# Kernel optimization log

Hardware: AMD Instinct MI355X
Metric: run time of the kernel (lower is better)

## Reference

```python
import jax, jax.numpy as jnp
import numpy as np

N, M, NNZ = 100000, 20000, 1000000
IN_C, OUT_C, HEADS, FH = 128, 128, 4, 32  # FH = hidden_channels // heads
NEG_SLOPE = 0.2


def setup_inputs() -> dict:
    key = jax.random.key(0)
    ks = jax.random.split(key, 10)
    def glorot(k, shape):
        fan_in, fan_out = shape[-1], shape[-2] if len(shape) > 1 else shape[-1]
        s = jnp.sqrt(6.0 / (fan_in + fan_out))
        return jax.random.uniform(k, shape, jnp.float32, -s, s)
    return {
        "x": jax.random.normal(ks[0], (N, IN_C), jnp.float32),
        "hyperedge_attr": jax.random.normal(ks[1], (M, IN_C), jnp.float32),
        "lin1_W": glorot(ks[2], (HEADS * FH, IN_C)),
        "he_lin1_W": glorot(ks[3], (HEADS * FH, IN_C)),
        "att1": glorot(ks[4], (1, HEADS, 2 * FH)),
        "bias1": jnp.zeros((HEADS * FH,), jnp.float32),
        "lin2_W": glorot(ks[5], (OUT_C, HEADS * FH)),
        "bias2": jnp.zeros((OUT_C,), jnp.float32),
        "node_idx": jax.random.randint(ks[6], (NNZ,), 0, N),
        "edge_idx": jax.random.randint(ks[7], (NNZ,), 0, M),
    }


def _seg_softmax(logits, seg, num_seg):
    # segment-wise softmax over entries grouped by seg (PyG softmax)
    m = jax.ops.segment_max(logits, seg, num_segments=num_seg)
    m = jnp.where(jnp.isfinite(m), m, 0.0)  # empty segments
    e = jnp.exp(logits - m[seg])
    s = jax.ops.segment_sum(e, seg, num_segments=num_seg)
    return e / (s[seg] + 1e-16)


def reference(x, hyperedge_attr, lin1_W, he_lin1_W, att1, bias1, lin2_W, bias2,
              node_idx, edge_idx):
    n, m, nnz = x.shape[0], hyperedge_attr.shape[0], node_idx.shape[0]
    ones = jnp.ones((nnz,), x.dtype)
    deg = jax.ops.segment_sum(ones, node_idx, num_segments=n)      # D
    Dinv = jnp.where(deg > 0, 1.0 / deg, 0.0)
    bsz = jax.ops.segment_sum(ones, edge_idx, num_segments=m)      # B
    Binv = jnp.where(bsz > 0, 1.0 / bsz, 0.0)

    # ---- layer 1: attention conv, heads=4, concat ----
    x1 = (x @ lin1_W.T).reshape(n, HEADS, FH)                      # [N,H,F]
    he = (hyperedge_attr @ he_lin1_W.T).reshape(m, HEADS, FH)      # [M,H,F]
    a_i = (x1[node_idx] * att1[:, :, :FH]).sum(-1)                 # [nnz,H]
    a_j = (he[edge_idx] * att1[:, :, FH:]).sum(-1)
    alpha = jax.nn.leaky_relu(a_i + a_j, NEG_SLOPE)
    alpha = _seg_softmax(alpha, node_idx, n)                        # softmax per node

    # node -> hyperedge: B[e] * alpha * x1[node]
    msg = Binv[edge_idx][:, None, None] * x1[node_idx] * alpha[:, :, None]
    out_e = jax.ops.segment_sum(msg, edge_idx, num_segments=m)      # [M,H,F]
    # hyperedge -> node: D[v] * alpha * out_e[edge]
    msg = Dinv[node_idx][:, None, None] * out_e[edge_idx] * alpha[:, :, None]
    out_n = jax.ops.segment_sum(msg, node_idx, num_segments=n)      # [N,H,F]
    h = jax.nn.elu(out_n.reshape(n, HEADS * FH) + bias1)            # HCHA applies elu

    # ---- layer 2: plain conv (heads=1) ----
    x2 = h @ lin2_W.T                                               # [N,OUT_C]
    oe = jax.ops.segment_sum(Binv[edge_idx][:, None] * x2[node_idx],
                             edge_idx, num_segments=m)
    out = jax.ops.segment_sum(Dinv[node_idx][:, None] * oe[edge_idx],
                              node_idx, num_segments=n)
    return out + bias2
```

## Files before the change

kernel.cpp:

```cpp
#include <hip/hip_runtime.h>
#include <cstdint>


#define E_SHIFT 6
#define N_SHIFT 7
#define EB_CAP 4096
#define NB_CAP 2048
#define PCHUNK 4096
#define NBE_CAP 320
#define NBN_CAP 800

__device__ __forceinline__ unsigned wave_incl_scan(unsigned x) {
#pragma unroll
  for (int s = 1; s < 64; s <<= 1) {
    unsigned t = __shfl_up(x, s, 64);
    if ((int)(threadIdx.x & 63) >= s) x += t;
  }
  return x;
}

__global__ __launch_bounds__(256) void bucket_count(const int* __restrict__ node_idx,
                                                    const int* __restrict__ edge_idx,
                                                    unsigned* __restrict__ bcnt_e,
                                                    unsigned* __restrict__ bcnt_n, int nnz) {
  __shared__ unsigned he[NBE_CAP];
  __shared__ unsigned hn[NBN_CAP];
  const int t = threadIdx.x;
  const int base = blockIdx.x * PCHUNK;
  const int cnt = min(PCHUNK, nnz - base);
  for (int b = t; b < NBE_CAP; b += 256) he[b] = 0;
  for (int b = t; b < NBN_CAP; b += 256) hn[b] = 0;
  __syncthreads();
  for (int idx = t; idx < cnt; idx += 256) {
    unsigned e = (unsigned)edge_idx[base + idx];
    unsigned n = (unsigned)node_idx[base + idx];
    atomicAdd(&he[e >> E_SHIFT], 1u);
    atomicAdd(&hn[n >> N_SHIFT], 1u);
  }
  __syncthreads();
  for (int b = t; b < NBE_CAP; b += 256) if (he[b]) atomicAdd(&bcnt_e[b], he[b]);
  for (int b = t; b < NBN_CAP; b += 256) if (hn[b]) atomicAdd(&bcnt_n[b], hn[b]);
}

__global__ __launch_bounds__(1024) void bucket_scan(const unsigned* __restrict__ bcnt_e,
                                                    const unsigned* __restrict__ bcnt_n,
                                                    unsigned* __restrict__ bbase_e,
                                                    unsigned* __restrict__ bcur_e,
                                                    unsigned* __restrict__ bbase_n,
                                                    unsigned* __restrict__ bcur_n,
                                                    unsigned* __restrict__ eoff,
                                                    unsigned* __restrict__ noff,
                                                    int nbe, int nbn, int M_, int N_, int nnz) {
  __shared__ unsigned wsum[16];
  const int i = threadIdx.x;
  const int lane = i & 63, wid = i >> 6;
  {
    unsigned v = (i < nbe) ? bcnt_e[i] : 0u;
    unsigned incl = wave_incl_scan(v);
    if (lane == 63) wsum[wid] = incl;
    __syncthreads();
    unsigned add = 0;
    for (int w = 0; w < wid; ++w) add += wsum[w];
    unsigned excl = add + incl - v;
    if (i <= nbe) bbase_e[i] = excl;
    if (i < nbe) bcur_e[i] = excl;
    __syncthreads();
  }
  {
    unsigned v = (i < nbn) ? bcnt_n[i] : 0u;
    unsigned incl = wave_incl_scan(v);
    if (lane == 63) wsum[wid] = incl;
    __syncthreads();
    unsigned add = 0;
    for (int w = 0; w < wid; ++w) add += wsum[w];
    unsigned excl = add + incl - v;
    if (i <= nbn) bbase_n[i] = excl;
    if (i < nbn) bcur_n[i] = excl;
  }
  if (i == 0) { eoff[M_] = (unsigned)nnz; noff[N_] = (unsigned)nnz; }
}

__global__ __launch_bounds__(256) void partition2(const int* __restrict__ node_idx,
                                                  const int* __restrict__ edge_idx,
                                                  unsigned* __restrict__ bcur_e,
                                                  unsigned* __restrict__ bcur_n,
                                                  unsigned* __restrict__ tmp_e,
                                                  unsigned* __restrict__ tmp_n, int nnz) {
  __shared__ unsigned he[NBE_CAP];
  __shared__ unsigned hn[NBN_CAP];
  const int t = threadIdx.x;
  const int base = blockIdx.x * PCHUNK;
  const int cnt = min(PCHUNK, nnz - base);

  for (int b = t; b < NBE_CAP; b += 256) he[b] = 0;
  for (int b = t; b < NBN_CAP; b += 256) hn[b] = 0;
  __syncthreads();

  for (int idx = t; idx < cnt; idx += 256) {
    unsigned e = (unsigned)edge_idx[base + idx];
    unsigned n = (unsigned)node_idx[base + idx];
    atomicAdd(&he[e >> E_SHIFT], 1u);
    atomicAdd(&hn[n >> N_SHIFT], 1u);
  }
  __syncthreads();

  for (int b = t; b < NBE_CAP; b += 256) {
    unsigned c = he[b];
    he[b] = c ? atomicAdd(&bcur_e[b], c) : 0u;
  }
  for (int b = t; b < NBN_CAP; b += 256) {
    unsigned c = hn[b];
    hn[b] = c ? atomicAdd(&bcur_n[b], c) : 0u;
  }
  __syncthreads();

  for (int idx = t; idx < cnt; idx += 256) {
    unsigned e = (unsigned)edge_idx[base + idx];
    unsigned n = (unsigned)node_idx[base + idx];
    unsigned pe = atomicAdd(&he[e >> E_SHIFT], 1u);
    tmp_e[pe] = ((e & 63u) << 17) | n;
    unsigned pn = atomicAdd(&hn[n >> N_SHIFT], 1u);
    tmp_n[pn] = ((n & 127u) << 15) | e;
  }
}

__device__ __forceinline__ float4 alpha4(const float* __restrict__ ai,
                                         const float* __restrict__ aj,
                                         unsigned n, unsigned e) {
  float4 av = *(const float4*)&ai[(size_t)n * 4];
  float4 bv = *(const float4*)&aj[(size_t)e * 4];
  float v0 = av.x + bv.x, v1 = av.y + bv.y, v2 = av.z + bv.z, v3 = av.w + bv.w;
  v0 = v0 > 0.f ? v0 : 0.2f * v0;
  v1 = v1 > 0.f ? v1 : 0.2f * v1;
  v2 = v2 > 0.f ? v2 : 0.2f * v2;
  v3 = v3 > 0.f ? v3 : 0.2f * v3;
  return make_float4(expf(v0), expf(v1), expf(v2), expf(v3));
}

__global__ __launch_bounds__(256) void sort_edge_exp(const unsigned* __restrict__ tmp,
                                                     const unsigned* __restrict__ bbase,
                                                     int M_,
                                                     const float* __restrict__ ai,
                                                     const float* __restrict__ aj,
                                                     float* __restrict__ ealpha_e,
                                                     int* __restrict__ enid,
                                                     unsigned* __restrict__ eoff,
                                                     float* __restrict__ binv) {
  __shared__ unsigned cur[64];
  __shared__ unsigned sbuf[EB_CAP];
  int b = blockIdx.x, t = threadIdx.x;
  int e0 = b << E_SHIFT;
  unsigned base = bbase[b];
  int cnt = (int)(bbase[b + 1] - base);
  if (t < 64) cur[t] = 0;
  __syncthreads();
  for (int idx = t; idx < cnt; idx += 256) {
    unsigned key = tmp[base + idx] >> 17;
    atomicAdd(&cur[key], 1u);
  }
  __syncthreads();
  {
    unsigned c = (t < 64) ? cur[t] : 0u;
    unsigned incl = wave_incl_scan(c);
    unsigned excl = incl - c;
    if (t < 64) {
      int e = e0 + t;
      if (e < M_) {
        eoff[e] = base + excl;
        binv[e] = c ? 1.f / (float)c : 0.f;
      }
      cur[t] = excl;
    }
  }
  __syncthreads();
  for (int idx = t; idx < cnt; idx += 256) {
    unsigned p = tmp[base + idx];
    unsigned key = p >> 17;
    unsigned pos = atomicAdd(&cur[key], 1u);
    if (pos < EB_CAP) {
      sbuf[pos] = p;
    } else {
      unsigned n = p & 0x1FFFFu;
      *(float4*)&ealpha_e[(size_t)(base + pos) * 4] = alpha4(ai, aj, n, e0 + key);
      enid[base + pos] = (int)n;
    }
  }
  __syncthreads();
  int lim = min(cnt, EB_CAP);
  for (int idx = t; idx < lim; idx += 256) {
    unsigned p = sbuf[idx];
    unsigned key = p >> 17, n = p & 0x1FFFFu;
    *(float4*)&ealpha_e[(size_t)(base + idx) * 4] = alpha4(ai, aj, n, e0 + key);
    enid[base + idx] = (int)n;
  }
}

__global__ __launch_bounds__(256) void sort_node_exp(const unsigned* __restrict__ tmp,
                                                     const unsigned* __restrict__ bbase,
                                                     int N_,
                                                     const float* __restrict__ ai,
                                                     const float* __restrict__ aj,
                                                     float* __restrict__ ealpha_n,
                                                     int* __restrict__ neid,
                                                     unsigned* __restrict__ noff,
                                                     float* __restrict__ dinv) {
  __shared__ unsigned cur[128];
  __shared__ unsigned sbuf[NB_CAP];
  __shared__ unsigned wtot;
  int b = blockIdx.x, t = threadIdx.x;
  int n0 = b << N_SHIFT;
  unsigned base = bbase[b];
  int cnt = (int)(bbase[b + 1] - base);
  if (t < 128) cur[t] = 0;
  __syncthreads();
  for (int idx = t; idx < cnt; idx += 256) {
    unsigned key = tmp[base + idx] >> 15;
    atomicAdd(&cur[key], 1u);
  }
  __syncthreads();
  {
    unsigned c = (t < 128) ? cur[t] : 0u;
    unsigned incl = wave_incl_scan(c);
    if (t == 63) wtot = incl;
    __syncthreads();
    unsigned excl = incl - c + ((t >= 64 && t < 128) ? wtot : 0u);
    if (t < 128) {
      int n = n0 + t;
      if (n < N_) {
        noff[n] = base + excl;
        dinv[n] = c ? 1.f / (float)c : 0.f;
      }
      cur[t] = excl;
    }
  }
  __syncthreads();
  for (int idx = t; idx < cnt; idx += 256) {
    unsigned p = tmp[base + idx];
    unsigned key = p >> 15;
    unsigned pos = atomicAdd(&cur[key], 1u);
    if (pos < NB_CAP) {
      sbuf[pos] = p;
    } else {
      unsigned e = p & 0x7FFFu;
      *(float4*)&ealpha_n[(size_t)(base + pos) * 4] = alpha4(ai, aj, n0 + key, e);
      neid[base + pos] = (int)e;
    }
  }
  __syncthreads();
  int lim = min(cnt, NB_CAP);
  for (int idx = t; idx < lim; idx += 256) {
    unsigned p = sbuf[idx];
    unsigned key = p >> 15, e = p & 0x7FFFu;
    *(float4*)&ealpha_n[(size_t)(base + idx) * 4] = alpha4(ai, aj, n0 + key, e);
    neid[base + idx] = (int)e;
  }
}

__global__ __launch_bounds__(256) void node_denom2(const unsigned* __restrict__ noff,
                                                   const float* __restrict__ ealpha_n,
                                                   float* __restrict__ rden, int N) {
  int v = blockIdx.x * 256 + threadIdx.x;
  if (v >= N) return;
  unsigned s = noff[v], en = noff[v + 1];
  float x = 0.f, y = 0.f, z = 0.f, w = 0.f;
  for (unsigned j = s; j < en; ++j) {
    float4 a = *(const float4*)&ealpha_n[(size_t)j * 4];
    x += a.x; y += a.y; z += a.z; w += a.w;
  }
  *(float4*)&rden[(size_t)v * 4] = make_float4(1.f / (x + 1e-16f), 1.f / (y + 1e-16f),
                                               1.f / (z + 1e-16f), 1.f / (w + 1e-16f));
}

__global__ __launch_bounds__(256) void wtrans(const float* __restrict__ W,
                                              float* __restrict__ WT) {
  int idx = blockIdx.x * 256 + threadIdx.x;
  if (idx >= 128 * 128) return;
  int k = idx >> 7, o = idx & 127;
  WT[idx] = W[o * 128 + k];
}

#define GM 64
__global__ __launch_bounds__(256) void gemm128t(const float* __restrict__ A,
                                                const float* __restrict__ WT,
                                                float* __restrict__ C, int rows,
                                                const float* __restrict__ att,
                                                float* __restrict__ aiout) {
  __shared__ __align__(16) float Ast[GM][132];
  const int tid = threadIdx.x;
  const int row0 = blockIdx.x * GM;

  for (int idx = tid; idx < GM * 32; idx += 256) {
    int r = idx >> 5, kq = idx & 31;
    int gr = row0 + r;
    float4 v = (gr < rows) ? *(const float4*)&A[(size_t)gr * 128 + kq * 4]
                           : make_float4(0.f, 0.f, 0.f, 0.f);
    *(float4*)&Ast[r][kq * 4] = v;
  }
  __syncthreads();

  const int tr = tid >> 5, tc = tid & 31;
  const int r0 = tr * 8, c0 = tc * 4;
  float acc[8][4] = {{0.f}};

  for (int k = 0; k < 128; k += 4) {
    float4 b0 = *(const float4*)&WT[(k + 0) * 128 + c0];
    float4 b1 = *(const float4*)&WT[(k + 1) * 128 + c0];
    float4 b2 = *(const float4*)&WT[(k + 2) * 128 + c0];
    float4 b3 = *(const float4*)&WT[(k + 3) * 128 + c0];
#pragma unroll
    for (int i = 0; i < 8; ++i) {
      float4 a = *(const float4*)&Ast[r0 + i][k];
      acc[i][0] += a.x * b0.x; acc[i][1] += a.x * b0.y; acc[i][2] += a.x * b0.z; acc[i][3] += a.x * b0.w;
      acc[i][0] += a.y * b1.x; acc[i][1] += a.y * b1.y; acc[i][2] += a.y * b1.z; acc[i][3] += a.y * b1.w;
      acc[i][0] += a.z * b2.x; acc[i][1] += a.z * b2.y; acc[i][2] += a.z * b2.z; acc[i][3] += a.z * b2.w;
      acc[i][0] += a.w * b3.x; acc[i][1] += a.w * b3.y; acc[i][2] += a.w * b3.z; acc[i][3] += a.w * b3.w;
    }
  }

#pragma unroll
  for (int i = 0; i < 8; ++i) {
    int gr = row0 + r0 + i;
    if (gr < rows)
      *(float4*)&C[(size_t)gr * 128 + c0] = make_float4(acc[i][0], acc[i][1], acc[i][2], acc[i][3]);
  }

  if (att) {
    int h = tc >> 3;
    float4 w = *(const float4*)&att[h * 64 + (c0 & 31)];
#pragma unroll
    for (int i = 0; i < 8; ++i) {
      float p = acc[i][0] * w.x + acc[i][1] * w.y + acc[i][2] * w.z + acc[i][3] * w.w;
      p += __shfl_xor(p, 1);
      p += __shfl_xor(p, 2);
      p += __shfl_xor(p, 4);
      if ((tc & 7) == 0) {
        int gr = row0 + r0 + i;
        if (gr < rows) aiout[(size_t)gr * 4 + h] = p;
      }
    }
  }
}

__global__ __launch_bounds__(256) void make_u(const float* __restrict__ W_he,
                                              const float* __restrict__ att1,
                                              float* __restrict__ u) {
  int idx = blockIdx.x * 256 + threadIdx.x;
  if (idx >= 512) return;
  int h = idx >> 7, k = idx & 127;
  float s = 0.f;
#pragma unroll
  for (int f = 0; f < 32; ++f)
    s += att1[h * 64 + 32 + f] * W_he[(size_t)(h * 32 + f) * 128 + k];
  u[h * 128 + k] = s;
}

__global__ __launch_bounds__(256) void att_dot_full(const float* __restrict__ feat,
                                                    const float* __restrict__ u,
                                                    float* __restrict__ outv, int rows) {
  int idx = blockIdx.x * 256 + threadIdx.x;
  if (idx >= rows * 4) return;
  int v = idx >> 2, h = idx & 3;
  const float4* fp = (const float4*)(feat + (size_t)v * 128);
  const float4* up = (const float4*)(u + h * 128);
  float s = 0.f;
#pragma unroll
  for (int q = 0; q < 32; ++q) {
    float4 a = up[q], f = fp[q];
    s += a.x * f.x + a.y * f.y + a.z * f.z + a.w * f.w;
  }
  outv[idx] = s;
}

#define ECH 256
__global__ __launch_bounds__(128) void edge_aggregate1(const float* __restrict__ x1,
                                                       const float* __restrict__ ealpha_e,
                                                       const float* __restrict__ rden,
                                                       const float* __restrict__ binv,
                                                       const int* __restrict__ enid,
                                                       const unsigned* __restrict__ eoff,
                                                       float* __restrict__ out_e) {
  __shared__ int nid[ECH];
  __shared__ float wal[ECH][4];
  int e = blockIdx.x, t = threadIdx.x, h = t >> 5;
  unsigned s = eoff[e], en = eoff[e + 1];
  float a0 = 0.f, a1 = 0.f, a2 = 0.f, a3 = 0.f;
  float a4 = 0.f, a5 = 0.f, a6 = 0.f, a7 = 0.f;
  for (unsigned base = s; base < en; base += ECH) {
    int cnt = (int)min((unsigned)ECH, en - base);
    __syncthreads();
    for (int c = t; c < cnt; c += 128) {
      int n = enid[base + c];
      nid[c] = n;
      float4 ea = *(const float4*)&ealpha_e[(size_t)(base + c) * 4];
      float4 rd = *(const float4*)&rden[(size_t)n * 4];
      wal[c][0] = ea.x * rd.x; wal[c][1] = ea.y * rd.y;
      wal[c][2] = ea.z * rd.z; wal[c][3] = ea.w * rd.w;
    }
    __syncthreads();
    int c = 0;
    for (; c + 8 <= cnt; c += 8) {
      a0 += wal[c + 0][h] * x1[(size_t)nid[c + 0] * 128 + t];
      a1 += wal[c + 1][h] * x1[(size_t)nid[c + 1] * 128 + t];
      a2 += wal[c + 2][h] * x1[(size_t)nid[c + 2] * 128 + t];
      a3 += wal[c + 3][h] * x1[(size_t)nid[c + 3] * 128 + t];
      a4 += wal[c + 4][h] * x1[(size_t)nid[c + 4] * 128 + t];
      a5 += wal[c + 5][h] * x1[(size_t)nid[c + 5] * 128 + t];
      a6 += wal[c + 6][h] * x1[(size_t)nid[c + 6] * 128 + t];
      a7 += wal[c + 7][h] * x1[(size_t)nid[c + 7] * 128 + t];
    }
    for (; c < cnt; ++c) a0 += wal[c][h] * x1[(size_t)nid[c] * 128 + t];
  }
  out_e[(size_t)e * 128 + t] = binv[e] * (((a0 + a1) + (a2 + a3)) + ((a4 + a5) + (a6 + a7)));
}

__global__ __launch_bounds__(128) void node_aggregate1(const float* __restrict__ out_e,
                                                       const float* __restrict__ ealpha_n,
                                                       const float* __restrict__ rden,
                                                       const float* __restrict__ dinv,
                                                       const float* __restrict__ bias1,
                                                       const int* __restrict__ neid,
                                                       const unsigned* __restrict__ noff,
                                                       float* __restrict__ hout) {
  int v = blockIdx.x, t = threadIdx.x, h = t >> 5;
  unsigned s = noff[v], en = noff[v + 1];
  float rd = dinv[v] * rden[v * 4 + h];
  float a0 = 0.f, a1 = 0.f, a2 = 0.f, a3 = 0.f;
  unsigned j = s;
  for (; j + 4 <= en; j += 4) {
    int e0 = neid[j], e1 = neid[j + 1], e2 = neid[j + 2], e3 = neid[j + 3];
    a0 += ealpha_n[(size_t)j * 4 + h] * out_e[(size_t)e0 * 128 + t];
    a1 += ealpha_n[(size_t)(j + 1) * 4 + h] * out_e[(size_t)e1 * 128 + t];
    a2 += ealpha_n[(size_t)(j + 2) * 4 + h] * out_e[(size_t)e2 * 128 + t];
    a3 += ealpha_n[(size_t)(j + 3) * 4 + h] * out_e[(size_t)e3 * 128 + t];
  }
  for (; j < en; ++j)
    a0 += ealpha_n[(size_t)j * 4 + h] * out_e[(size_t)neid[j] * 128 + t];
  float val = rd * (a0 + a1 + a2 + a3) + bias1[t];
  hout[(size_t)v * 128 + t] = val > 0.f ? val : expm1f(val);
}

__global__ __launch_bounds__(128) void edge_aggregate2(const float* __restrict__ hfeat,
                                                       const float* __restrict__ binv,
                                                       const int* __restrict__ enid,
                                                       const unsigned* __restrict__ eoff,
                                                       float* __restrict__ oe) {
  __shared__ int nid[ECH];
  int e = blockIdx.x, t = threadIdx.x;
  unsigned s = eoff[e], en = eoff[e + 1];
  float a0 = 0.f, a1 = 0.f, a2 = 0.f, a3 = 0.f;
  float a4 = 0.f, a5 = 0.f, a6 = 0.f, a7 = 0.f;
  for (unsigned base = s; base < en; base += ECH) {
    int cnt = (int)min((unsigned)ECH, en - base);
    __syncthreads();
    for (int c = t; c < cnt; c += 128) nid[c] = enid[base + c];
    __syncthreads();
    int c = 0;
    for (; c + 8 <= cnt; c += 8) {
      a0 += hfeat[(size_t)nid[c + 0] * 128 + t];
      a1 += hfeat[(size_t)nid[c + 1] * 128 + t];
      a2 += hfeat[(size_t)nid[c + 2] * 128 + t];
      a3 += hfeat[(size_t)nid[c + 3] * 128 + t];
      a4 += hfeat[(size_t)nid[c + 4] * 128 + t];
      a5 += hfeat[(size_t)nid[c + 5] * 128 + t];
      a6 += hfeat[(size_t)nid[c + 6] * 128 + t];
      a7 += hfeat[(size_t)nid[c + 7] * 128 + t];
    }
    for (; c < cnt; ++c) a0 += hfeat[(size_t)nid[c] * 128 + t];
  }
  oe[(size_t)e * 128 + t] = binv[e] * (((a0 + a1) + (a2 + a3)) + ((a4 + a5) + (a6 + a7)));
}

__global__ __launch_bounds__(128) void node_aggregate2(const float* __restrict__ oe2,
                                                       const float* __restrict__ dinv,
                                                       const float* __restrict__ bias2,
                                                       const int* __restrict__ neid,
                                                       const unsigned* __restrict__ noff,
                                                       float* __restrict__ out) {
  int v = blockIdx.x, t = threadIdx.x;
  unsigned s = noff[v], en = noff[v + 1];
  float a0 = 0.f, a1 = 0.f, a2 = 0.f, a3 = 0.f;
  unsigned j = s;
  for (; j + 4 <= en; j += 4) {
    int e0 = neid[j], e1 = neid[j + 1], e2 = neid[j + 2], e3 = neid[j + 3];
    a0 += oe2[(size_t)e0 * 128 + t];
    a1 += oe2[(size_t)e1 * 128 + t];
    a2 += oe2[(size_t)e2 * 128 + t];
    a3 += oe2[(size_t)e3 * 128 + t];
  }
  for (; j < en; ++j) a0 += oe2[(size_t)neid[j] * 128 + t];
  out[(size_t)v * 128 + t] = dinv[v] * (a0 + a1 + a2 + a3) + bias2[t];
}

extern "C" void kernel_launch(void* const* d_in, const int* in_sizes, int n_in,
                              void* d_out, int out_size, void* d_ws, size_t ws_size,
                              hipStream_t stream) {
  (void)n_in; (void)out_size; (void)ws_size;
  const float* x      = (const float*)d_in[0];
  const float* hea    = (const float*)d_in[1];
  const float* lin1W  = (const float*)d_in[2];
  const float* helinW = (const float*)d_in[3];
  const float* att1   = (const float*)d_in[4];
  const float* bias1  = (const float*)d_in[5];
  const float* lin2W  = (const float*)d_in[6];
  const float* bias2  = (const float*)d_in[7];
  const int* node_idx = (const int*)d_in[8];
  const int* edge_idx = (const int*)d_in[9];
  float* out = (float*)d_out;

  const int N   = in_sizes[0] / 128;
  const int M   = in_sizes[1] / 128;
  const int NNZ = in_sizes[8];
  const int NBE = (M + 63) >> E_SHIFT;
  const int NBN = (N + 127) >> N_SHIFT;

  char* base = (char*)d_ws;
  size_t off = 0;
  auto alloc = [&](size_t bytes) -> char* {
    char* p = base + off;
    off = (off + bytes + 255) & ~(size_t)255;
    return p;
  };
  float* x1    = (float*)alloc((size_t)N * 128 * 4);
  float* hbuf  = (float*)alloc((size_t)N * 128 * 4);
  float* heoe  = (float*)alloc((size_t)M * 128 * 4);
  float* ai    = (float*)alloc((size_t)N * 4 * 4);
  float* aj    = (float*)alloc((size_t)M * 4 * 4);
  float* u     = (float*)alloc(512 * 4);
  float* WT1   = (float*)alloc(128 * 128 * 4);
  float* WT2   = (float*)alloc(128 * 128 * 4);
  float* dinv  = (float*)alloc((size_t)N * 4);
  float* binv  = (float*)alloc((size_t)M * 4);
  float* rden  = (float*)alloc((size_t)N * 4 * 4);
  char* zstart = base + off;
  unsigned* bcnt_e = (unsigned*)alloc((size_t)NBE * 4);
  unsigned* bcnt_n = (unsigned*)alloc((size_t)NBN * 4);
  size_t zbytes = (size_t)((base + off) - zstart);
  float* ealpha_e = (float*)alloc((size_t)NNZ * 4 * 4);
  float* ealpha_n = (float*)alloc((size_t)NNZ * 4 * 4);
  unsigned* tmp_e = (unsigned*)alloc((size_t)NNZ * 4);
  unsigned* tmp_n = (unsigned*)alloc((size_t)NNZ * 4);
  unsigned* noff  = (unsigned*)alloc((size_t)(N + 1) * 4);
  unsigned* eoff  = (unsigned*)alloc((size_t)(M + 1) * 4);
  unsigned* bbase_e = (unsigned*)alloc((size_t)(NBE + 1) * 4);
  unsigned* bbase_n = (unsigned*)alloc((size_t)(NBN + 1) * 4);
  unsigned* bcur_e = (unsigned*)alloc((size_t)NBE * 4);
  unsigned* bcur_n = (unsigned*)alloc((size_t)NBN * 4);
  int* enid       = (int*)alloc((size_t)NNZ * 4);
  int* neid       = (int*)alloc((size_t)NNZ * 4);

  hipMemsetAsync(zstart, 0, zbytes, stream);

  const int g_pchunk = (NNZ + PCHUNK - 1) / PCHUNK;
  bucket_count<<<g_pchunk, 256, 0, stream>>>(node_idx, edge_idx, bcnt_e, bcnt_n, NNZ);
  bucket_scan<<<1, 1024, 0, stream>>>(bcnt_e, bcnt_n, bbase_e, bcur_e, bbase_n, bcur_n,
                                      eoff, noff, NBE, NBN, M, N, NNZ);
  partition2<<<g_pchunk, 256, 0, stream>>>(node_idx, edge_idx, bcur_e, bcur_n,
                                           tmp_e, tmp_n, NNZ);

  wtrans<<<64, 256, 0, stream>>>(lin1W, WT1);
  wtrans<<<64, 256, 0, stream>>>(lin2W, WT2);
  gemm128t<<<(N + GM - 1) / GM, 256, 0, stream>>>(x, WT1, x1, N, att1, ai);
  make_u<<<2, 256, 0, stream>>>(helinW, att1, u);
  att_dot_full<<<(M * 4 + 255) / 256, 256, 0, stream>>>(hea, u, aj, M);

  sort_edge_exp<<<NBE, 256, 0, stream>>>(tmp_e, bbase_e, M, ai, aj, ealpha_e, enid,
                                         eoff, binv);
  sort_node_exp<<<NBN, 256, 0, stream>>>(tmp_n, bbase_n, N, ai, aj, ealpha_n, neid,
                                         noff, dinv);
  node_denom2<<<(N + 255) / 256, 256, 0, stream>>>(noff, ealpha_n, rden, N);

  edge_aggregate1<<<M, 128, 0, stream>>>(x1, ealpha_e, rden, binv, enid, eoff, heoe);
  node_aggregate1<<<N, 128, 0, stream>>>(heoe, ealpha_n, rden, dinv, bias1, neid, noff, hbuf);

  edge_aggregate2<<<M, 128, 0, stream>>>(hbuf, binv, enid, eoff, heoe);
  gemm128t<<<(M + GM - 1) / GM, 256, 0, stream>>>(heoe, WT2, x1, M, nullptr, nullptr);
  node_aggregate2<<<N, 128, 0, stream>>>(x1, dinv, bias2, neid, noff, out);
}
```

Measured before the change: 488.7 us.

## Fold softmax denominator and Binv into edge alphas; use float4 multi-row gather aggregation

The edge-sort kernel now runs after the node denominator pass and writes final edge weights (exp * 1/denom * Binv), so edge_aggregate1 no longer stages weights in shared memory or reads rden and binv. All four aggregation kernels are rewritten so each 32-lane group handles every fourth incident row, using float4 loads over the 128 features and a shared-memory reduction across the four groups. This is meant to cut per-row gather instructions and shared-memory staging and to raise memory-level parallelism. The cost is a final cross-wave reduction, plus moving the edge sort later in the chain, which adds a dependency on rden.

```diff
diff --git a/kernel.cpp b/kernel.cpp
--- a/kernel.cpp
+++ b/kernel.cpp
@@ -137,64 +137,6 @@
   return make_float4(expf(v0), expf(v1), expf(v2), expf(v3));
 }
 
-__global__ __launch_bounds__(256) void sort_edge_exp(const unsigned* __restrict__ tmp,
-                                                     const unsigned* __restrict__ bbase,
-                                                     int M_,
-                                                     const float* __restrict__ ai,
-                                                     const float* __restrict__ aj,
-                                                     float* __restrict__ ealpha_e,
-                                                     int* __restrict__ enid,
-                                                     unsigned* __restrict__ eoff,
-                                                     float* __restrict__ binv) {
-  __shared__ unsigned cur[64];
-  __shared__ unsigned sbuf[EB_CAP];
-  int b = blockIdx.x, t = threadIdx.x;
-  int e0 = b << E_SHIFT;
-  unsigned base = bbase[b];
-  int cnt = (int)(bbase[b + 1] - base);
-  if (t < 64) cur[t] = 0;
-  __syncthreads();
-  for (int idx = t; idx < cnt; idx += 256) {
-    unsigned key = tmp[base + idx] >> 17;
-    atomicAdd(&cur[key], 1u);
-  }
-  __syncthreads();
-  {
-    unsigned c = (t < 64) ? cur[t] : 0u;
-    unsigned incl = wave_incl_scan(c);
-    unsigned excl = incl - c;
-    if (t < 64) {
-      int e = e0 + t;
-      if (e < M_) {
-        eoff[e] = base + excl;
-        binv[e] = c ? 1.f / (float)c : 0.f;
-      }
-      cur[t] = excl;
-    }
-  }
-  __syncthreads();
-  for (int idx = t; idx < cnt; idx += 256) {
-    unsigned p = tmp[base + idx];
-    unsigned key = p >> 17;
-    unsigned pos = atomicAdd(&cur[key], 1u);
-    if (pos < EB_CAP) {
-      sbuf[pos] = p;
-    } else {
-      unsigned n = p & 0x1FFFFu;
-      *(float4*)&ealpha_e[(size_t)(base + pos) * 4] = alpha4(ai, aj, n, e0 + key);
-      enid[base + pos] = (int)n;
-    }
-  }
-  __syncthreads();
-  int lim = min(cnt, EB_CAP);
-  for (int idx = t; idx < lim; idx += 256) {
-    unsigned p = sbuf[idx];
-    unsigned key = p >> 17, n = p & 0x1FFFFu;
-    *(float4*)&ealpha_e[(size_t)(base + idx) * 4] = alpha4(ai, aj, n, e0 + key);
-    enid[base + idx] = (int)n;
-  }
-}
-
 __global__ __launch_bounds__(256) void sort_node_exp(const unsigned* __restrict__ tmp,
                                                      const unsigned* __restrict__ bbase,
                                                      int N_,
@@ -271,6 +213,76 @@
                                                1.f / (z + 1e-16f), 1.f / (w + 1e-16f));
 }
 
+__global__ __launch_bounds__(256) void sort_edge_exp(const unsigned* __restrict__ tmp,
+                                                     const unsigned* __restrict__ bbase,
+                                                     int M_,
+                                                     const float* __restrict__ ai,
+                                                     const float* __restrict__ aj,
+                                                     const float* __restrict__ rden,
+                                                     float* __restrict__ alpha_e,
+                                                     int* __restrict__ enid,
+                                                     unsigned* __restrict__ eoff,
+                                                     float* __restrict__ binv) {
+  __shared__ unsigned cur[64];
+  __shared__ float binv_s[64];
+  __shared__ unsigned sbuf[EB_CAP];
+  int b = blockIdx.x, t = threadIdx.x;
+  int e0 = b << E_SHIFT;
+  unsigned base = bbase[b];
+  int cnt = (int)(bbase[b + 1] - base);
+  if (t < 64) cur[t] = 0;
+  __syncthreads();
+  for (int idx = t; idx < cnt; idx += 256) {
+    unsigned key = tmp[base + idx] >> 17;
+    atomicAdd(&cur[key], 1u);
+  }
+  __syncthreads();
+  {
+    unsigned c = (t < 64) ? cur[t] : 0u;
+    unsigned incl = wave_incl_scan(c);
+    unsigned excl = incl - c;
+    if (t < 64) {
+      float bv = c ? 1.f / (float)c : 0.f;
+      binv_s[t] = bv;
+      int e = e0 + t;
+      if (e < M_) {
+        eoff[e] = base + excl;
+        binv[e] = bv;
+      }
+      cur[t] = excl;
+    }
+  }
+  __syncthreads();
+  for (int idx = t; idx < cnt; idx += 256) {
+    unsigned p = tmp[base + idx];
+    unsigned key = p >> 17;
+    unsigned pos = atomicAdd(&cur[key], 1u);
+    if (pos < EB_CAP) {
+      sbuf[pos] = p;
+    } else {
+      unsigned n = p & 0x1FFFFu;
+      float4 al = alpha4(ai, aj, n, e0 + key);
+      float4 rd = *(const float4*)&rden[(size_t)n * 4];
+      float bv = binv_s[key];
+      *(float4*)&alpha_e[(size_t)(base + pos) * 4] =
+          make_float4(al.x * rd.x * bv, al.y * rd.y * bv, al.z * rd.z * bv, al.w * rd.w * bv);
+      enid[base + pos] = (int)n;
+    }
+  }
+  __syncthreads();
+  int lim = min(cnt, EB_CAP);
+  for (int idx = t; idx < lim; idx += 256) {
+    unsigned p = sbuf[idx];
+    unsigned key = p >> 17, n = p & 0x1FFFFu;
+    float4 al = alpha4(ai, aj, n, e0 + key);
+    float4 rd = *(const float4*)&rden[(size_t)n * 4];
+    float bv = binv_s[key];
+    *(float4*)&alpha_e[(size_t)(base + idx) * 4] =
+        make_float4(al.x * rd.x * bv, al.y * rd.y * bv, al.z * rd.z * bv, al.w * rd.w * bv);
+    enid[base + idx] = (int)n;
+  }
+}
+
 __global__ __launch_bounds__(256) void wtrans(const float* __restrict__ W,
                                               float* __restrict__ WT) {
   int idx = blockIdx.x * 256 + threadIdx.x;
@@ -371,46 +383,43 @@
   outv[idx] = s;
 }
 
-#define ECH 256
 __global__ __launch_bounds__(128) void edge_aggregate1(const float* __restrict__ x1,
-                                                       const float* __restrict__ ealpha_e,
-                                                       const float* __restrict__ rden,
-                                                       const float* __restrict__ binv,
+                                                       const float* __restrict__ alpha_e,
                                                        const int* __restrict__ enid,
                                                        const unsigned* __restrict__ eoff,
                                                        float* __restrict__ out_e) {
-  __shared__ int nid[ECH];
-  __shared__ float wal[ECH][4];
-  int e = blockIdx.x, t = threadIdx.x, h = t >> 5;
-  unsigned s = eoff[e], en = eoff[e + 1];
-  float a0 = 0.f, a1 = 0.f, a2 = 0.f, a3 = 0.f;
-  float a4 = 0.f, a5 = 0.f, a6 = 0.f, a7 = 0.f;
-  for (unsigned base = s; base < en; base += ECH) {
-    int cnt = (int)min((unsigned)ECH, en - base);
-    __syncthreads();
-    for (int c = t; c < cnt; c += 128) {
-      int n = enid[base + c];
-      nid[c] = n;
-      float4 ea = *(const float4*)&ealpha_e[(size_t)(base + c) * 4];
-      float4 rd = *(const float4*)&rden[(size_t)n * 4];
-      wal[c][0] = ea.x * rd.x; wal[c][1] = ea.y * rd.y;
-      wal[c][2] = ea.z * rd.z; wal[c][3] = ea.w * rd.w;
-    }
-    __syncthreads();
-    int c = 0;
-    for (; c + 8 <= cnt; c += 8) {
-      a0 += wal[c + 0][h] * x1[(size_t)nid[c + 0] * 128 + t];
-      a1 += wal[c + 1][h] * x1[(size_t)nid[c + 1] * 128 + t];
-      a2 += wal[c + 2][h] * x1[(size_t)nid[c + 2] * 128 + t];
-      a3 += wal[c + 3][h] * x1[(size_t)nid[c + 3] * 128 + t];
-      a4 += wal[c + 4][h] * x1[(size_t)nid[c + 4] * 128 + t];
-      a5 += wal[c + 5][h] * x1[(size_t)nid[c + 5] * 128 + t];
-      a6 += wal[c + 6][h] * x1[(size_t)nid[c + 6] * 128 + t];
-      a7 += wal[c + 7][h] * x1[(size_t)nid[c + 7] * 128 + t];
-    }
-    for (; c < cnt; ++c) a0 += wal[c][h] * x1[(size_t)nid[c] * 128 + t];
-  }
-  out_e[(size_t)e * 128 + t] = binv[e] * (((a0 + a1) + (a2 + a3)) + ((a4 + a5) + (a6 + a7)));
+  __shared__ float red[4][128];
+  const int e = blockIdx.x, t = threadIdx.x;
+  const int q = t >> 5, l = t & 31, hh = l >> 3;
+  const unsigned s = eoff[e], en = eoff[e + 1];
+  float4 A0 = make_float4(0.f, 0.f, 0.f, 0.f), A1 = A0, A2 = A0, A3 = A0;
+  unsigned j = s + q;
+  for (; j + 12 < en; j += 16) {
+    int n0 = enid[j], n1 = enid[j + 4], n2 = enid[j + 8], n3 = enid[j + 12];
+    float w0 = alpha_e[(size_t)j * 4 + hh];
+    float w1 = alpha_e[(size_t)(j + 4) * 4 + hh];
+    float w2 = alpha_e[(size_t)(j + 8) * 4 + hh];
+    float w3 = alpha_e[(size_t)(j + 12) * 4 + hh];
+    float4 a0 = *(const float4*)&x1[(size_t)n0 * 128 + l * 4];
+    float4 a1 = *(const float4*)&x1[(size_t)n1 * 128 + l * 4];
+    float4 a2 = *(const float4*)&x1[(size_t)n2 * 128 + l * 4];
+    float4 a3 = *(const float4*)&x1[(size_t)n3 * 128 + l * 4];
+    A0.x += w0 * a0.x; A0.y += w0 * a0.y; A0.z += w0 * a0.z; A0.w += w0 * a0.w;
+    A1.x += w1 * a1.x; A1.y += w1 * a1.y; A1.z += w1 * a1.z; A1.w += w1 * a1.w;
+    A2.x += w2 * a2.x; A2.y += w2 * a2.y; A2.z += w2 * a2.z; A2.w += w2 * a2.w;
+    A3.x += w3 * a3.x; A3.y += w3 * a3.y; A3.z += w3 * a3.z; A3.w += w3 * a3.w;
+  }
+  for (; j < en; j += 4) {
+    int n = enid[j];
+    float w = alpha_e[(size_t)j * 4 + hh];
+    float4 a = *(const float4*)&x1[(size_t)n * 128 + l * 4];
+    A0.x += w * a.x; A0.y += w * a.y; A0.z += w * a.z; A0.w += w * a.w;
+  }
+  float4 A = make_float4((A0.x + A1.x) + (A2.x + A3.x), (A0.y + A1.y) + (A2.y + A3.y),
+                         (A0.z + A1.z) + (A2.z + A3.z), (A0.w + A1.w) + (A2.w + A3.w));
+  *(float4*)&red[q][l * 4] = A;
+  __syncthreads();
+  out_e[(size_t)e * 128 + t] = red[0][t] + red[1][t] + red[2][t] + red[3][t];
 }
 
 __global__ __launch_bounds__(128) void node_aggregate1(const float* __restrict__ out_e,
@@ -421,21 +430,32 @@
                                                        const int* __restrict__ neid,
                                                        const unsigned* __restrict__ noff,
                                                        float* __restrict__ hout) {
-  int v = blockIdx.x, t = threadIdx.x, h = t >> 5;
-  unsigned s = noff[v], en = noff[v + 1];
-  float rd = dinv[v] * rden[v * 4 + h];
-  float a0 = 0.f, a1 = 0.f, a2 = 0.f, a3 = 0.f;
-  unsigned j = s;
-  for (; j + 4 <= en; j += 4) {
-    int e0 = neid[j], e1 = neid[j + 1], e2 = neid[j + 2], e3 = neid[j + 3];
-    a0 += ealpha_n[(size_t)j * 4 + h] * out_e[(size_t)e0 * 128 + t];
-    a1 += ealpha_n[(size_t)(j + 1) * 4 + h] * out_e[(size_t)e1 * 128 + t];
-    a2 += ealpha_n[(size_t)(j + 2) * 4 + h] * out_e[(size_t)e2 * 128 + t];
-    a3 += ealpha_n[(size_t)(j + 3) * 4 + h] * out_e[(size_t)e3 * 128 + t];
-  }
-  for (; j < en; ++j)
-    a0 += ealpha_n[(size_t)j * 4 + h] * out_e[(size_t)neid[j] * 128 + t];
-  float val = rd * (a0 + a1 + a2 + a3) + bias1[t];
+  __shared__ float red[4][128];
+  const int v = blockIdx.x, t = threadIdx.x;
+  const int q = t >> 5, l = t & 31, hh = l >> 3;
+  const unsigned s = noff[v], en = noff[v + 1];
+  float4 A0 = make_float4(0.f, 0.f, 0.f, 0.f), A1 = A0;
+  unsigned j = s + q;
+  for (; j + 4 < en; j += 8) {
+    int e0 = neid[j], e1 = neid[j + 4];
+    float w0 = ealpha_n[(size_t)j * 4 + hh];
+    float w1 = ealpha_n[(size_t)(j + 4) * 4 + hh];
+    float4 a0 = *(const float4*)&out_e[(size_t)e0 * 128 + l * 4];
+    float4 a1 = *(const float4*)&out_e[(size_t)e1 * 128 + l * 4];
+    A0.x += w0 * a0.x; A0.y += w0 * a0.y; A0.z += w0 * a0.z; A0.w += w0 * a0.w;
+    A1.x += w1 * a1.x; A1.y += w1 * a1.y; A1.z += w1 * a1.z; A1.w += w1 * a1.w;
+  }
+  for (; j < en; j += 4) {
+    int e0 = neid[j];
+    float w = ealpha_n[(size_t)j * 4 + hh];
+    float4 a = *(const float4*)&out_e[(size_t)e0 * 128 + l * 4];
+    A0.x += w * a.x; A0.y += w * a.y; A0.z += w * a.z; A0.w += w * a.w;
+  }
+  float4 A = make_float4(A0.x + A1.x, A0.y + A1.y, A0.z + A1.z, A0.w + A1.w);
+  *(float4*)&red[q][l * 4] = A;
+  __syncthreads();
+  float rd = dinv[v] * rden[(size_t)v * 4 + (t >> 5)];
+  float val = rd * (red[0][t] + red[1][t] + red[2][t] + red[3][t]) + bias1[t];
   hout[(size_t)v * 128 + t] = val > 0.f ? val : expm1f(val);
 }
 
@@ -444,30 +464,33 @@
                                                        const int* __restrict__ enid,
                                                        const unsigned* __restrict__ eoff,
                                                        float* __restrict__ oe) {
-  __shared__ int nid[ECH];
-  int e = blockIdx.x, t = threadIdx.x;
-  unsigned s = eoff[e], en = eoff[e + 1];
-  float a0 = 0.f, a1 = 0.f, a2 = 0.f, a3 = 0.f;
-  float a4 = 0.f, a5 = 0.f, a6 = 0.f, a7 = 0.f;
-  for (unsigned base = s; base < en; base += ECH) {
-    int cnt = (int)min((unsigned)ECH, en - base);
-    __syncthreads();
-    for (int c = t; c < cnt; c += 128) nid[c] = enid[base + c];
-    __syncthreads();
-    int c = 0;
-    for (; c + 8 <= cnt; c += 8) {
-      a0 += hfeat[(size_t)nid[c + 0] * 128 + t];
-      a1 += hfeat[(size_t)nid[c + 1] * 128 + t];
-      a2 += hfeat[(size_t)nid[c + 2] * 128 + t];
-      a3 += hfeat[(size_t)nid[c + 3] * 128 + t];
-      a4 += hfeat[(size_t)nid[c + 4] * 128 + t];
-      a5 += hfeat[(size_t)nid[c + 5] * 128 + t];
-      a6 += hfeat[(size_t)nid[c + 6] * 128 + t];
-      a7 += hfeat[(size_t)nid[c + 7] * 128 + t];
-    }
-    for (; c < cnt; ++c) a0 += hfeat[(size_t)nid[c] * 128 + t];
-  }
-  oe[(size_t)e * 128 + t] = binv[e] * (((a0 + a1) + (a2 + a3)) + ((a4 + a5) + (a6 + a7)));
+  __shared__ float red[4][128];
+  const int e = blockIdx.x, t = threadIdx.x;
+  const int q = t >> 5, l = t & 31;
+  const unsigned s = eoff[e], en = eoff[e + 1];
+  float4 A0 = make_float4(0.f, 0.f, 0.f, 0.f), A1 = A0, A2 = A0, A3 = A0;
+  unsigned j = s + q;
+  for (; j + 12 < en; j += 16) {
+    int n0 = enid[j], n1 = enid[j + 4], n2 = enid[j + 8], n3 = enid[j + 12];
+    float4 a0 = *(const float4*)&hfeat[(size_t)n0 * 128 + l * 4];
+    float4 a1 = *(const float4*)&hfeat[(size_t)n1 * 128 + l * 4];
+    float4 a2 = *(const float4*)&hfeat[(size_t)n2 * 128 + l * 4];
+    float4 a3 = *(const float4*)&hfeat[(size_t)n3 * 128 + l * 4];
+    A0.x += a0.x; A0.y += a0.y; A0.z += a0.z; A0.w += a0.w;
+    A1.x += a1.x; A1.y += a1.y; A1.z += a1.z; A1.w += a1.w;
+    A2.x += a2.x; A2.y += a2.y; A2.z += a2.z; A2.w += a2.w;
+    A3.x += a3.x; A3.y += a3.y; A3.z += a3.z; A3.w += a3.w;
+  }
+  for (; j < en; j += 4) {
+    int n = enid[j];
+    float4 a = *(const float4*)&hfeat[(size_t)n * 128 + l * 4];
+    A0.x += a.x; A0.y += a.y; A0.z += a.z; A0.w += a.w;
+  }
+  float4 A = make_float4((A0.x + A1.x) + (A2.x + A3.x), (A0.y + A1.y) + (A2.y + A3.y),
+                         (A0.z + A1.z) + (A2.z + A3.z), (A0.w + A1.w) + (A2.w + A3.w));
+  *(float4*)&red[q][l * 4] = A;
+  __syncthreads();
+  oe[(size_t)e * 128 + t] = binv[e] * (red[0][t] + red[1][t] + red[2][t] + red[3][t]);
 }
 
 __global__ __launch_bounds__(128) void node_aggregate2(const float* __restrict__ oe2,
@@ -476,19 +499,28 @@
                                                        const int* __restrict__ neid,
                                                        const unsigned* __restrict__ noff,
                                                        float* __restrict__ out) {
-  int v = blockIdx.x, t = threadIdx.x;
-  unsigned s = noff[v], en = noff[v + 1];
-  float a0 = 0.f, a1 = 0.f, a2 = 0.f, a3 = 0.f;
-  unsigned j = s;
-  for (; j + 4 <= en; j += 4) {
-    int e0 = neid[j], e1 = neid[j + 1], e2 = neid[j + 2], e3 = neid[j + 3];
-    a0 += oe2[(size_t)e0 * 128 + t];
-    a1 += oe2[(size_t)e1 * 128 + t];
-    a2 += oe2[(size_t)e2 * 128 + t];
-    a3 += oe2[(size_t)e3 * 128 + t];
-  }
-  for (; j < en; ++j) a0 += oe2[(size_t)neid[j] * 128 + t];
-  out[(size_t)v * 128 + t] = dinv[v] * (a0 + a1 + a2 + a3) + bias2[t];
+  __shared__ float red[4][128];
+  const int v = blockIdx.x, t = threadIdx.x;
+  const int q = t >> 5, l = t & 31;
+  const unsigned s = noff[v], en = noff[v + 1];
+  float4 A0 = make_float4(0.f, 0.f, 0.f, 0.f), A1 = A0;
+  unsigned j = s + q;
+  for (; j + 4 < en; j += 8) {
+    int e0 = neid[j], e1 = neid[j + 4];
+    float4 a0 = *(const float4*)&oe2[(size_t)e0 * 128 + l * 4];
+    float4 a1 = *(const float4*)&oe2[(size_t)e1 * 128 + l * 4];
+    A0.x += a0.x; A0.y += a0.y; A0.z += a0.z; A0.w += a0.w;
+    A1.x += a1.x; A1.y += a1.y; A1.z += a1.z; A1.w += a1.w;
+  }
+  for (; j < en; j += 4) {
+    int e0 = neid[j];
+    float4 a = *(const float4*)&oe2[(size_t)e0 * 128 + l * 4];
+    A0.x += a.x; A0.y += a.y; A0.z += a.z; A0.w += a.w;
+  }
+  float4 A = make_float4(A0.x + A1.x, A0.y + A1.y, A0.z + A1.z, A0.w + A1.w);
+  *(float4*)&red[q][l * 4] = A;
+  __syncthreads();
+  out[(size_t)v * 128 + t] = dinv[v] * (red[0][t] + red[1][t] + red[2][t] + red[3][t]) + bias2[t];
 }
 
 extern "C" void kernel_launch(void* const* d_in, const int* in_sizes, int n_in,
@@ -535,7 +567,7 @@
   unsigned* bcnt_e = (unsigned*)alloc((size_t)NBE * 4);
   unsigned* bcnt_n = (unsigned*)alloc((size_t)NBN * 4);
   size_t zbytes = (size_t)((base + off) - zstart);
-  float* ealpha_e = (float*)alloc((size_t)NNZ * 4 * 4);
+  float* alpha_e  = (float*)alloc((size_t)NNZ * 4 * 4);
   float* ealpha_n = (float*)alloc((size_t)NNZ * 4 * 4);
   unsigned* tmp_e = (unsigned*)alloc((size_t)NNZ * 4);
   unsigned* tmp_n = (unsigned*)alloc((size_t)NNZ * 4);
@@ -563,13 +595,13 @@
   make_u<<<2, 256, 0, stream>>>(helinW, att1, u);
   att_dot_full<<<(M * 4 + 255) / 256, 256, 0, stream>>>(hea, u, aj, M);
 
-  sort_edge_exp<<<NBE, 256, 0, stream>>>(tmp_e, bbase_e, M, ai, aj, ealpha_e, enid,
-                                         eoff, binv);
   sort_node_exp<<<NBN, 256, 0, stream>>>(tmp_n, bbase_n, N, ai, aj, ealpha_n, neid,
                                          noff, dinv);
   node_denom2<<<(N + 255) / 256, 256, 0, stream>>>(noff, ealpha_n, rden, N);
-
-  edge_aggregate1<<<M, 128, 0, stream>>>(x1, ealpha_e, rden, binv, enid, eoff, heoe);
+  sort_edge_exp<<<NBE, 256, 0, stream>>>(tmp_e, bbase_e, M, ai, aj, rden, alpha_e, enid,
+                                         eoff, binv);
+
+  edge_aggregate1<<<M, 128, 0, stream>>>(x1, alpha_e, enid, eoff, heoe);
   node_aggregate1<<<N, 128, 0, stream>>>(heoe, ealpha_n, rden, dinv, bias1, neid, noff, hbuf);
 
   edge_aggregate2<<<M, 128, 0, stream>>>(hbuf, binv, enid, eoff, heoe);
```

After: 470.1 us, median of 2. 1.04x faster.
